# Kernel tuning notes

Hardware: AMD Instinct MI355X
Metric: run time of the kernel (lower is better)

## Reference

```python
import jax, jax.numpy as jnp
import numpy as np

N = 50000
E = 800000
IN = 256
HID = 64
HEADS = 4
EPS = 1e-5


def batchnorm(x, g, b):
    # training-mode BatchNorm1d over node dim, biased variance (torch semantics)
    mu = jnp.mean(x, axis=0)
    var = jnp.mean((x - mu) ** 2, axis=0)
    return (x - mu) * jax.lax.rsqrt(var + EPS) * g + b


def gat(x, edge_index, W, a_src, a_dst, bias, heads, out_ch, num_nodes):
    src, dst = edge_index[0], edge_index[1]
    h = (x @ W).reshape(num_nodes, heads, out_ch)          # [N,H,C]
    al_s = jnp.einsum('nhc,hc->nh', h, a_src)              # [N,H]
    al_d = jnp.einsum('nhc,hc->nh', h, a_dst)
    e = jax.nn.leaky_relu(al_s[src] + al_d[dst], 0.2)      # [E,H]
    # segment softmax over destination neighborhoods
    m = jax.ops.segment_max(e, dst, num_segments=num_nodes)
    m = jnp.where(jnp.isfinite(m), m, 0.0)
    ex = jnp.exp(e - m[dst])                               # [E,H]
    denom = jax.ops.segment_sum(ex, dst, num_segments=num_nodes)
    alpha = ex / (denom[dst] + 1e-16)                      # [E,H]
    msg = alpha[:, :, None] * h[src]                       # [E,H,C]
    out = jax.ops.segment_sum(msg, dst, num_segments=num_nodes)
    return out.reshape(num_nodes, heads * out_ch) + bias


def setup_inputs() -> dict:
    key = jax.random.key(0)
    ks = jax.random.split(key, 12)
    d = {}
    d['x'] = jax.random.normal(ks[0], (N, IN), jnp.float32)
    d['edge_index'] = jax.random.randint(ks[1], (2, E), 0, N, jnp.int32)
    d['bn1_g'] = jnp.ones((IN,), jnp.float32)
    d['bn1_b'] = jnp.zeros((IN,), jnp.float32)
    d['lin1_W'] = jax.random.normal(ks[2], (IN, HID * HEADS), jnp.float32) * (1.0 / np.sqrt(IN))
    d['lin1_b'] = jnp.zeros((HID * HEADS,), jnp.float32)
    d['con1_W'] = jax.random.normal(ks[3], (IN, HID * HEADS), jnp.float32) * (1.0 / np.sqrt(IN))
    d['con1_asrc'] = jax.random.normal(ks[4], (HEADS, HID), jnp.float32) * 0.1
    d['con1_adst'] = jax.random.normal(ks[5], (HEADS, HID), jnp.float32) * 0.1
    d['con1_b'] = jnp.zeros((HID * HEADS,), jnp.float32)
    d['bn3_g'] = jnp.ones((HID * HEADS,), jnp.float32)
    d['bn3_b'] = jnp.zeros((HID * HEADS,), jnp.float32)
    d['lin3_W'] = jax.random.normal(ks[6], (HID * HEADS, 2), jnp.float32) * (1.0 / np.sqrt(HID * HEADS))
    d['lin3_b'] = jnp.zeros((2,), jnp.float32)
    d['con3_W'] = jax.random.normal(ks[7], (HID * HEADS, 2), jnp.float32) * (1.0 / np.sqrt(HID * HEADS))
    d['con3_asrc'] = jax.random.normal(ks[8], (1, 2), jnp.float32) * 0.1
    d['con3_adst'] = jax.random.normal(ks[9], (1, 2), jnp.float32) * 0.1
    d['con3_b'] = jnp.zeros((2,), jnp.float32)
    return d


def reference(x, edge_index, bn1_g, bn1_b, lin1_W, lin1_b, con1_W, con1_asrc, con1_adst, con1_b,
              bn3_g, bn3_b, lin3_W, lin3_b, con3_W, con3_asrc, con3_adst, con3_b):
    x = batchnorm(x, bn1_g, bn1_b)
    x = jax.nn.relu(x @ lin1_W + lin1_b
                    + gat(x, edge_index, con1_W, con1_asrc, con1_adst, con1_b, HEADS, HID, N))
    x = batchnorm(x, bn3_g, bn3_b)
    x = jax.nn.relu(x @ lin3_W + lin3_b
                    + gat(x, edge_index, con3_W, con3_asrc, con3_adst, con3_b, 1, 2, N))
    return x
```

## Files before the change

kernel.cpp:

```cpp
#include <hip/hip_runtime.h>
#include <math.h>

#define NN 50000
#define NE 800000
#define IC 256
#define EPS 1e-5f

typedef __attribute__((ext_vector_type(8))) short short8;
typedef __attribute__((ext_vector_type(4))) float f32x4;

enum : int {
  OFF_S1     = 0,
  OFF_S2     = 256,
  OFF_COUNTS = 512,
  ZERO_END   = OFF_COUNTS + 50000,
  OFF_CURSOR = ZERO_END,
  OFF_START  = OFF_CURSOR + 50000,
  OFF_BSUM   = OFF_START + 50004,
  OFF_BOFF   = OFF_BSUM + 64,
  OFF_ALS    = OFF_BOFF + 64,
  OFF_ALD    = OFF_ALS + 200000,
  OFF_SRCS   = OFF_ALD + 200000,
  OFF_Y32    = OFF_SRCS + 800000,
  OFF_ND4    = OFF_Y32 + 100000,
  OFF_BFH    = OFF_ND4 + 200000,
  OFF_HBF    = OFF_BFH + 65536,
  OFF_YLBF   = OFF_HBF + 6400000,
  WS_FLOATS  = OFF_YLBF + 6400000
};

__device__ __forceinline__ float lrelu(float s) { return s > 0.f ? s : 0.2f * s; }
__device__ __forceinline__ float b2f(unsigned short u) {
  return __uint_as_float(((unsigned)u) << 16);
}
__device__ __forceinline__ unsigned short f2bf(float f) {
  unsigned u = __float_as_uint(f);
  return (unsigned short)((u + 0x7fffu + ((u >> 16) & 1u)) >> 16);
}
__device__ __forceinline__ unsigned cvtpk(float lo, float hi) {
  unsigned r;
  asm("v_cvt_pk_bf16_f32 %0, %1, %2" : "=v"(r) : "v"(lo), "v"(hi));
  return r;
}

__global__ __launch_bounds__(256) void k_prep(const float* __restrict__ x,
                                              float* __restrict__ S1,
                                              float* __restrict__ S2,
                                              const int* __restrict__ dst,
                                              int* __restrict__ counts,
                                              const float* __restrict__ Wlin,
                                              const float* __restrict__ Wcon,
                                              unsigned short* __restrict__ Bfh) {
  int b = blockIdx.x;
  if (b < 1024) {
    int c = threadIdx.x;
    float s1 = 0.f, s2 = 0.f;
    for (int r = b; r < NN; r += 1024) {
      float v = x[r * IC + c];
      s1 += v;
      s2 = fmaf(v, v, s2);
    }
    atomicAdd(&S1[c], s1);
    atomicAdd(&S2[c], s2);
  } else if (b < 4149) {
    int e = (b - 1024) * 256 + threadIdx.x;
    atomicAdd(&counts[dst[e]], 1);
  } else {
    int id = (b - 4149) * 256 + threadIdx.x;
    int j = id & 7, lane = (id >> 3) & 63, nt = (id >> 9) & 31, ks = id >> 14;
    int k = ks * 32 + ((lane >> 4) << 3) + j;
    int n = nt * 16 + (lane & 15);
    float v = (n < 256) ? Wlin[k * 256 + n] : Wcon[k * 256 + (n - 256)];
    Bfh[id] = f2bf(v);
  }
}

__global__ __launch_bounds__(256) void k_bnstats2(const unsigned short* __restrict__ x1,
                                                  float* __restrict__ S1,
                                                  float* __restrict__ S2) {
  int c = threadIdx.x;
  float s1 = 0.f, s2 = 0.f;
  for (int r = blockIdx.x; r < NN; r += gridDim.x) {
    float v = b2f(x1[r * IC + c]);
    s1 += v;
    s2 = fmaf(v, v, s2);
  }
  atomicAdd(&S1[c], s1);
  atomicAdd(&S2[c], s2);
}

__global__ __launch_bounds__(256, 4) void k_gemm(const float* __restrict__ x,
                                                 const float* __restrict__ S1,
                                                 const float* __restrict__ S2,
                                                 const float* __restrict__ bng,
                                                 const float* __restrict__ bnb,
                                                 const unsigned short* __restrict__ Bfh,
                                                 unsigned short* __restrict__ ylbf,
                                                 unsigned short* __restrict__ hbf,
                                                 const float* __restrict__ asrc,
                                                 const float* __restrict__ adst,
                                                 float* __restrict__ als,
                                                 float* __restrict__ ald,
                                                 const int* __restrict__ counts,
                                                 int* __restrict__ start,
                                                 int* __restrict__ cursor) {
  const int tid = threadIdx.x;
  const int b = blockIdx.x;
  if (b < 56) {
    if (b >= 49) return;
    __shared__ int red[4], wsum[4];
    const int lane = tid & 63, wv = tid >> 6;
    const int base = b << 10;
    int pre = 0;
    for (int i = tid; i < base; i += 256) pre += counts[i];
#pragma unroll
    for (int off = 1; off < 64; off <<= 1) pre += __shfl_xor(pre, off, 64);
    if (lane == 0) red[wv] = pre;
    const int i0 = base + tid * 4;
    int c0 = (i0 < NN) ? counts[i0] : 0;
    int c1 = (i0 + 1 < NN) ? counts[i0 + 1] : 0;
    int c2 = (i0 + 2 < NN) ? counts[i0 + 2] : 0;
    int c3 = (i0 + 3 < NN) ? counts[i0 + 3] : 0;
    const int tsum = c0 + c1 + c2 + c3;
    int isc = tsum;
#pragma unroll
    for (int off = 1; off < 64; off <<= 1) {
      int t = __shfl_up(isc, off, 64);
      if (lane >= off) isc += t;
    }
    if (lane == 63) wsum[wv] = isc;
    __syncthreads();
    int ex = red[0] + red[1] + red[2] + red[3] + (isc - tsum);
    for (int w = 0; w < wv; ++w) ex += wsum[w];
    if (i0 < NN) { start[i0] = ex; cursor[i0] = ex; }
    ex += c0;
    if (i0 + 1 < NN) { start[i0 + 1] = ex; cursor[i0 + 1] = ex; }
    ex += c1;
    if (i0 + 2 < NN) { start[i0 + 2] = ex; cursor[i0 + 2] = ex; }
    ex += c2;
    if (i0 + 3 < NN) { start[i0 + 3] = ex; cursor[i0 + 3] = ex; }
    ex += c3;
    if (b == 48 && tid == 255) start[NN] = ex;
    return;
  }
  const int g = b - 56;
  const int row_blk = (g >> 4) * 8 + (g & 7);
  const int bn = (g >> 3) & 1;
  if (row_blk >= 782) return;
  const int row0 = row_blk * 64;
  __shared__ unsigned short Ah[2048];
  __shared__ float sc[256], sh[256];
  const int wave = tid >> 6, lane = tid & 63;
  {
    float mu = S1[tid] * (1.f / NN);
    float var = S2[tid] * (1.f / NN) - mu * mu;
    float ss = bng[tid] / sqrtf(var + EPS);
    sc[tid] = ss;
    sh[tid] = bnb[tid] - mu * ss;
  }
  const float4* x4 = (const float4*)x;
  const short8* Bh8 = (const short8*)Bfh;
  f32x4 acc[4][4];
#pragma unroll
  for (int i = 0; i < 4; ++i)
#pragma unroll
    for (int j = 0; j < 4; ++j) acc[i][j] = (f32x4){0.f, 0.f, 0.f, 0.f};

  const int m = tid >> 2, kg = tid & 3;
  const int r = row0 + m;
  const int aaddr = (((m >> 4) * 64) + ((m & 15) | (kg << 4))) * 8;
  __syncthreads();

  for (int ks = 0; ks < 8; ++ks) {
    const int c0 = ks * 32 + kg * 8;
    float v[8];
    if (r < NN) {
      int base = (r * IC + c0) >> 2;
      float4 fa = x4[base], fb = x4[base + 1];
      v[0] = fa.x; v[1] = fa.y; v[2] = fa.z; v[3] = fa.w;
      v[4] = fb.x; v[5] = fb.y; v[6] = fb.z; v[7] = fb.w;
#pragma unroll
      for (int j = 0; j < 8; ++j) v[j] = fmaf(v[j], sc[c0 + j], sh[c0 + j]);
    } else {
#pragma unroll
      for (int j = 0; j < 8; ++j) v[j] = 0.f;
    }
    unsigned ph[4];
#pragma unroll
    for (int j = 0; j < 4; ++j) ph[j] = cvtpk(v[2 * j], v[2 * j + 1]);
    *(uint4*)&Ah[aaddr] = make_uint4(ph[0], ph[1], ph[2], ph[3]);
    __syncthreads();

    short8 ah[4];
#pragma unroll
    for (int mt = 0; mt < 4; ++mt)
      ah[mt] = *(const short8*)&Ah[(mt * 64 + lane) * 8];
#pragma unroll
    for (int nt = 0; nt < 4; ++nt) {
      short8 bh = Bh8[(ks * 32 + bn * 16 + wave * 4 + nt) * 64 + lane];
#pragma unroll
      for (int mt = 0; mt < 4; ++mt)
        acc[mt][nt] = __builtin_amdgcn_mfma_f32_16x16x32_bf16(ah[mt], bh, acc[mt][nt], 0, 0, 0);
    }
    __syncthreads();
  }
  const int colq = lane & 15, quad = lane >> 4;
  if (bn == 0) {
#pragma unroll
    for (int mt = 0; mt < 4; ++mt)
#pragma unroll
      for (int reg = 0; reg < 4; ++reg) {
        int rr = row0 + mt * 16 + quad * 4 + reg;
        if (rr < NN) {
#pragma unroll
          for (int nt = 0; nt < 4; ++nt)
            ylbf[rr * IC + wave * 64 + nt * 16 + colq] = f2bf(acc[mt][nt][reg]);
        }
      }
  } else {
    const int head = wave;
    float asv[4], adv[4];
#pragma unroll
    for (int j = 0; j < 4; ++j) {
      asv[j] = asrc[head * 64 + j * 16 + colq];
      adv[j] = adst[head * 64 + j * 16 + colq];
    }
#pragma unroll
    for (int mt = 0; mt < 4; ++mt)
#pragma unroll
      for (int reg = 0; reg < 4; ++reg) {
        int rr = row0 + mt * 16 + quad * 4 + reg;
        float sA = 0.f, dA = 0.f;
#pragma unroll
        for (int j = 0; j < 4; ++j) {
          float hA = acc[mt][j][reg];
          sA = fmaf(hA, asv[j], sA);
          dA = fmaf(hA, adv[j], dA);
          if (rr < NN) hbf[rr * IC + head * 64 + j * 16 + colq] = f2bf(hA);
        }
#pragma unroll
        for (int off = 1; off < 16; off <<= 1) {
          sA += __shfl_xor(sA, off, 64);
          dA += __shfl_xor(dA, off, 64);
        }
        if (rr < NN) {
          if (colq == 0) als[rr * 4 + head] = sA;
          else if (colq == 1) ald[rr * 4 + head] = dA;
        }
      }
  }
}

__global__ __launch_bounds__(256) void k_scatter(const int* __restrict__ src,
                                                 const int* __restrict__ dst,
                                                 int* __restrict__ cursor,
                                                 int* __restrict__ srcs,
                                                 float* __restrict__ S1,
                                                 float* __restrict__ S2) {
  if (blockIdx.x == 0) {
    S1[threadIdx.x] = 0.f;
    S2[threadIdx.x] = 0.f;
  }
  int e = blockIdx.x * 256 + threadIdx.x;
  int pos = atomicAdd(&cursor[dst[e]], 1);
  srcs[pos] = src[e];
}

__global__ __launch_bounds__(256) void k_agg(const ushort4* __restrict__ hq,
                                             ushort4* __restrict__ x1,
                                             const float4* __restrict__ als4,
                                             const float4* __restrict__ ald4,
                                             const int* __restrict__ start,
                                             const int* __restrict__ srcs,
                                             const float4* __restrict__ lb4,
                                             const float4* __restrict__ cb4,
                                             const int nb0) {
  __shared__ float lsp[1024];
  const int tid = threadIdx.x;
  const int wave = tid >> 6, lane = tid & 63, head = lane >> 4;
  const int n = nb0 + blockIdx.x * 4 + wave;
  const float* als = (const float*)als4;
  const int s = start[n], t = start[n + 1];
  const int deg = t - s;
  const float4 aldv = ald4[n];
  int svk = -1;
  float p0 = 0.f, p1 = 0.f, p2 = 0.f, p3 = 0.f;
  if (lane < deg) {
    svk = srcs[s + lane];
    float4 a = als4[svk];
    p0 = __expf(lrelu(a.x + aldv.x));
    p1 = __expf(lrelu(a.y + aldv.y));
    p2 = __expf(lrelu(a.z + aldv.z));
    p3 = __expf(lrelu(a.w + aldv.w));
  }
  *(float4*)&lsp[wave * 256 + lane * 4] = make_float4(p0, p1, p2, p3);
  float d0 = p0, d1 = p1, d2 = p2, d3 = p3;
  const float aldh = head == 0 ? aldv.x : head == 1 ? aldv.y : head == 2 ? aldv.z : aldv.w;
  if (deg > 64) {
    for (int i = s + 64 + lane; i < t; i += 64) {
      float4 a = als4[srcs[i]];
      d0 += __expf(lrelu(a.x + aldv.x));
      d1 += __expf(lrelu(a.y + aldv.y));
      d2 += __expf(lrelu(a.z + aldv.z));
      d3 += __expf(lrelu(a.w + aldv.w));
    }
  }
#pragma unroll
  for (int off = 1; off < 64; off <<= 1) {
    d0 += __shfl_xor(d0, off, 64);
    d1 += __shfl_xor(d1, off, 64);
    d2 += __shfl_xor(d2, off, 64);
    d3 += __shfl_xor(d3, off, 64);
  }
  const float inv =
      1.f / ((head == 0 ? d0 : head == 1 ? d1 : head == 2 ? d2 : d3) + 1e-16f);
  float a0 = 0.f, a1 = 0.f, a2 = 0.f, a3 = 0.f;
  const int cnt = min(deg, 64);
  const int wbase = wave * 256 + head;
  int j = 0;
  for (; j + 4 <= cnt; j += 4) {
    int sv0 = __shfl(svk, j, 64), sv1 = __shfl(svk, j + 1, 64);
    int sv2 = __shfl(svk, j + 2, 64), sv3 = __shfl(svk, j + 3, 64);
    ushort4 hv0 = hq[sv0 * 64 + lane];
    ushort4 hv1 = hq[sv1 * 64 + lane];
    ushort4 hv2 = hq[sv2 * 64 + lane];
    ushort4 hv3 = hq[sv3 * 64 + lane];
    float w0 = lsp[wbase + j * 4], w1 = lsp[wbase + j * 4 + 4];
    float w2 = lsp[wbase + j * 4 + 8], w3 = lsp[wbase + j * 4 + 12];
    a0 = fmaf(w0, b2f(hv0.x), a0); a1 = fmaf(w0, b2f(hv0.y), a1);
    a2 = fmaf(w0, b2f(hv0.z), a2); a3 = fmaf(w0, b2f(hv0.w), a3);
    a0 = fmaf(w1, b2f(hv1.x), a0); a1 = fmaf(w1, b2f(hv1.y), a1);
    a2 = fmaf(w1, b2f(hv1.z), a2); a3 = fmaf(w1, b2f(hv1.w), a3);
    a0 = fmaf(w2, b2f(hv2.x), a0); a1 = fmaf(w2, b2f(hv2.y), a1);
    a2 = fmaf(w2, b2f(hv2.z), a2); a3 = fmaf(w2, b2f(hv2.w), a3);
    a0 = fmaf(w3, b2f(hv3.x), a0); a1 = fmaf(w3, b2f(hv3.y), a1);
    a2 = fmaf(w3, b2f(hv3.z), a2); a3 = fmaf(w3, b2f(hv3.w), a3);
  }
  for (; j < cnt; ++j) {
    int sv = __shfl(svk, j, 64);
    float w = lsp[wbase + j * 4];
    ushort4 hv = hq[sv * 64 + lane];
    a0 = fmaf(w, b2f(hv.x), a0);
    a1 = fmaf(w, b2f(hv.y), a1);
    a2 = fmaf(w, b2f(hv.z), a2);
    a3 = fmaf(w, b2f(hv.w), a3);
  }
  if (deg > 64) {
    for (int i = s + 64; i < t; ++i) {
      int sv = srcs[i];
      float av = als[sv * 4 + head];
      float p = __expf(lrelu(av + aldh));
      ushort4 hv = hq[sv * 64 + lane];
      a0 = fmaf(p, b2f(hv.x), a0);
      a1 = fmaf(p, b2f(hv.y), a1);
      a2 = fmaf(p, b2f(hv.z), a2);
      a3 = fmaf(p, b2f(hv.w), a3);
    }
  }
  ushort4 yb = x1[n * 64 + lane];
  float4 bb1 = lb4[lane], bb2 = cb4[lane];
  ushort4 rb;
  rb.x = f2bf(fmaxf(fmaf(a0, inv, b2f(yb.x) + bb1.x + bb2.x), 0.f));
  rb.y = f2bf(fmaxf(fmaf(a1, inv, b2f(yb.y) + bb1.y + bb2.y), 0.f));
  rb.z = f2bf(fmaxf(fmaf(a2, inv, b2f(yb.z) + bb1.z + bb2.z), 0.f));
  rb.w = f2bf(fmaxf(fmaf(a3, inv, b2f(yb.w) + bb1.w + bb2.w), 0.f));
  x1[n * 64 + lane] = rb;
}

__global__ __launch_bounds__(256) void k_node2(const ushort4* __restrict__ x1,
                                               const float* __restrict__ S1,
                                               const float* __restrict__ S2,
                                               const float* __restrict__ g3,
                                               const float* __restrict__ b3,
                                               const float4* __restrict__ Wl4,
                                               const float4* __restrict__ Wc4,
                                               const float* __restrict__ a3s,
                                               const float* __restrict__ a3d,
                                               const float* __restrict__ l3b,
                                               const float* __restrict__ c3b,
                                               float2* __restrict__ y32,
                                               float4* __restrict__ nd4) {
  __shared__ float sc[256], sh[256];
  const int tid = threadIdx.x;
  {
    float mu = S1[tid] * (1.f / NN);
    float var = S2[tid] * (1.f / NN) - mu * mu;
    float ss = g3[tid] / sqrtf(var + EPS);
    sc[tid] = ss;
    sh[tid] = b3[tid] - mu * ss;
  }
  __syncthreads();
  const int n = blockIdx.x * 4 + (tid >> 6);
  const int lane = tid & 63;
  ushort4 xb = x1[n * 64 + lane];
  float x0 = fmaf(b2f(xb.x), sc[lane * 4 + 0], sh[lane * 4 + 0]);
  float x1v = fmaf(b2f(xb.y), sc[lane * 4 + 1], sh[lane * 4 + 1]);
  float x2 = fmaf(b2f(xb.z), sc[lane * 4 + 2], sh[lane * 4 + 2]);
  float x3 = fmaf(b2f(xb.w), sc[lane * 4 + 3], sh[lane * 4 + 3]);
  float4 wa = Wl4[lane * 2], wb = Wl4[lane * 2 + 1];
  float y0 = x0 * wa.x + x1v * wa.z + x2 * wb.x + x3 * wb.z;
  float y1 = x0 * wa.y + x1v * wa.w + x2 * wb.y + x3 * wb.w;
  float4 ca = Wc4[lane * 2], cb = Wc4[lane * 2 + 1];
  float g0 = x0 * ca.x + x1v * ca.z + x2 * cb.x + x3 * cb.z;
  float g1 = x0 * ca.y + x1v * ca.w + x2 * cb.y + x3 * cb.w;
#pragma unroll
  for (int off = 1; off < 64; off <<= 1) {
    y0 += __shfl_xor(y0, off, 64);
    y1 += __shfl_xor(y1, off, 64);
    g0 += __shfl_xor(g0, off, 64);
    g1 += __shfl_xor(g1, off, 64);
  }
  if (lane == 0) {
    y32[n] = make_float2(y0 + l3b[0] + c3b[0], y1 + l3b[1] + c3b[1]);
    nd4[n] = make_float4(g0 * a3s[0] + g1 * a3s[1], g0, g1,
                         g0 * a3d[0] + g1 * a3d[1]);
  }
}

__global__ __launch_bounds__(256) void k_final(const int* __restrict__ start,
                                               const int* __restrict__ srcs,
                                               const float4* __restrict__ nd4,
                                               const float2* __restrict__ y32,
                                               float* __restrict__ out) {
  const int tid = threadIdx.x;
  const int n = blockIdx.x * 16 + (tid >> 4);
  const int li = tid & 15;
  const int s = start[n], t = start[n + 1];
  const float ad = nd4[n].w;
  float den = 0.f, a0 = 0.f, a1 = 0.f;
  for (int ii = s + li; ii < t; ii += 16) {
    float4 vv = nd4[srcs[ii]];
    float p = __expf(lrelu(vv.x + ad));
    den += p;
    a0 = fmaf(p, vv.y, a0);
    a1 = fmaf(p, vv.z, a1);
  }
#pragma unroll
  for (int off = 1; off < 16; off <<= 1) {
    den += __shfl_xor(den, off, 64);
    a0 += __shfl_xor(a0, off, 64);
    a1 += __shfl_xor(a1, off, 64);
  }
  if (li == 0) {
    float2 y = y32[n];
    float inv = 1.f / (den + 1e-16f);
    out[2 * n] = fmaxf(fmaf(a0, inv, y.x), 0.f);
    out[2 * n + 1] = fmaxf(fmaf(a1, inv, y.y), 0.f);
  }
}

extern "C" void kernel_launch(void* const* d_in, const int* in_sizes, int n_in,
                              void* d_out, int out_size, void* d_ws, size_t ws_size,
                              hipStream_t stream) {
  const float* x = (const float*)d_in[0];
  const int* ei = (const int*)d_in[1];
  const float* bn1_g = (const float*)d_in[2];
  const float* bn1_b = (const float*)d_in[3];
  const float* lin1_W = (const float*)d_in[4];
  const float* lin1_b = (const float*)d_in[5];
  const float* con1_W = (const float*)d_in[6];
  const float* con1_as = (const float*)d_in[7];
  const float* con1_ad = (const float*)d_in[8];
  const float* con1_b = (const float*)d_in[9];
  const float* bn3_g = (const float*)d_in[10];
  const float* bn3_b = (const float*)d_in[11];
  const float* lin3_W = (const float*)d_in[12];
  const float* lin3_b = (const float*)d_in[13];
  const float* con3_W = (const float*)d_in[14];
  const float* con3_as = (const float*)d_in[15];
  const float* con3_ad = (const float*)d_in[16];
  const float* con3_b = (const float*)d_in[17];
  float* ws = (float*)d_ws;
  const int* srcA = ei;
  const int* dstA = ei + NE;

  float* S1 = ws + OFF_S1;
  float* S2 = ws + OFF_S2;
  int* counts = (int*)(ws + OFF_COUNTS);
  int* cursor = (int*)(ws + OFF_CURSOR);
  int* start = (int*)(ws + OFF_START);
  float* als = ws + OFF_ALS;
  float* ald = ws + OFF_ALD;
  int* srcs = (int*)(ws + OFF_SRCS);
  float2* y32 = (float2*)(ws + OFF_Y32);
  float4* nd4 = (float4*)(ws + OFF_ND4);
  unsigned short* Bfh = (unsigned short*)(ws + OFF_BFH);
  unsigned short* hbf = (unsigned short*)(ws + OFF_HBF);
  unsigned short* ylbf = (unsigned short*)(ws + OFF_YLBF);

  hipMemsetAsync(ws, 0, (size_t)ZERO_END * sizeof(float), stream);

  k_prep<<<4661, 256, 0, stream>>>(x, S1, S2, dstA, counts, lin1_W, con1_W, Bfh);
  k_gemm<<<56 + 1568, 256, 0, stream>>>(x, S1, S2, bn1_g, bn1_b, Bfh, ylbf, hbf,
                                        con1_as, con1_ad, als, ald, counts, start,
                                        cursor);
  k_scatter<<<3125, 256, 0, stream>>>(srcA, dstA, cursor, srcs, S1, S2);
  k_agg<<<6250, 256, 0, stream>>>((const ushort4*)hbf, (ushort4*)ylbf,
                                  (const float4*)als, (const float4*)ald, start,
                                  srcs, (const float4*)lin1_b,
                                  (const float4*)con1_b, 0);
  k_agg<<<6250, 256, 0, stream>>>((const ushort4*)hbf, (ushort4*)ylbf,
                                  (const float4*)als, (const float4*)ald, start,
                                  srcs, (const float4*)lin1_b,
                                  (const float4*)con1_b, 25000);
  k_bnstats2<<<1024, 256, 0, stream>>>(ylbf, S1, S2);
  k_node2<<<12500, 256, 0, stream>>>((const ushort4*)ylbf, S1, S2, bn3_g, bn3_b,
                                     (const float4*)lin3_W, (const float4*)con3_W,
                                     con3_as, con3_ad, lin3_b, con3_b, y32, nd4);
  k_final<<<3125, 256, 0, stream>>>(start, srcs, nd4, y32, (float*)d_out);
}
```

Baseline: 407.7 us.

## Replace scatter-time atomics with privatized 8-way counts and per-edge ranks

Degree counting now uses 8 privatized count arrays selected by block index, and records each edge's rank from the atomicAdd return value. The scan builds per-copy offsets, so the scatter computes positions directly without a second round of atomics on the cursor. This aims to reduce atomic contention and drop the atomics from the scatter. In exchange the scan reads 8x more count data, the memset zeroes a larger region, and an extra byte-per-edge rank array is stored. The bnstats2 grid is also halved.

```diff
diff --git a/kernel.cpp b/kernel.cpp
--- a/kernel.cpp
+++ b/kernel.cpp
@@ -5,6 +5,7 @@
 #define NE 800000
 #define IC 256
 #define EPS 1e-5f
+#define P8 50176
 
 typedef __attribute__((ext_vector_type(8))) short short8;
 typedef __attribute__((ext_vector_type(4))) float f32x4;
@@ -12,13 +13,12 @@
 enum : int {
   OFF_S1     = 0,
   OFF_S2     = 256,
-  OFF_COUNTS = 512,
-  ZERO_END   = OFF_COUNTS + 50000,
-  OFF_CURSOR = ZERO_END,
-  OFF_START  = OFF_CURSOR + 50000,
-  OFF_BSUM   = OFF_START + 50004,
-  OFF_BOFF   = OFF_BSUM + 64,
-  OFF_ALS    = OFF_BOFF + 64,
+  OFF_C8     = 512,
+  ZERO_END   = OFF_C8 + 8 * P8,
+  OFF_COFF   = ZERO_END,
+  OFF_START  = OFF_COFF + 8 * P8,
+  OFF_RANK   = OFF_START + 50004,
+  OFF_ALS    = OFF_RANK + 200000,
   OFF_ALD    = OFF_ALS + 200000,
   OFF_SRCS   = OFF_ALD + 200000,
   OFF_Y32    = OFF_SRCS + 800000,
@@ -47,7 +47,8 @@
                                               float* __restrict__ S1,
                                               float* __restrict__ S2,
                                               const int* __restrict__ dst,
-                                              int* __restrict__ counts,
+                                              int* __restrict__ counts8,
+                                              unsigned char* __restrict__ rank8,
                                               const float* __restrict__ Wlin,
                                               const float* __restrict__ Wcon,
                                               unsigned short* __restrict__ Bfh) {
@@ -64,7 +65,9 @@
     atomicAdd(&S2[c], s2);
   } else if (b < 4149) {
     int e = (b - 1024) * 256 + threadIdx.x;
-    atomicAdd(&counts[dst[e]], 1);
+    int copy = b & 7;
+    int old = atomicAdd(&counts8[copy * P8 + dst[e]], 1);
+    rank8[e] = (unsigned char)old;
   } else {
     int id = (b - 4149) * 256 + threadIdx.x;
     int j = id & 7, lane = (id >> 3) & 63, nt = (id >> 9) & 31, ks = id >> 14;
@@ -101,9 +104,9 @@
                                                  const float* __restrict__ adst,
                                                  float* __restrict__ als,
                                                  float* __restrict__ ald,
-                                                 const int* __restrict__ counts,
-                                                 int* __restrict__ start,
-                                                 int* __restrict__ cursor) {
+                                                 const int* __restrict__ counts8,
+                                                 int* __restrict__ coff,
+                                                 int* __restrict__ start) {
   const int tid = threadIdx.x;
   const int b = blockIdx.x;
   if (b < 56) {
@@ -112,16 +115,31 @@
     const int lane = tid & 63, wv = tid >> 6;
     const int base = b << 10;
     int pre = 0;
-    for (int i = tid; i < base; i += 256) pre += counts[i];
+    for (int i = tid; i < base; i += 256) {
+      int s = 0;
+#pragma unroll
+      for (int k = 0; k < 8; ++k) s += counts8[k * P8 + i];
+      pre += s;
+    }
 #pragma unroll
     for (int off = 1; off < 64; off <<= 1) pre += __shfl_xor(pre, off, 64);
     if (lane == 0) red[wv] = pre;
     const int i0 = base + tid * 4;
-    int c0 = (i0 < NN) ? counts[i0] : 0;
-    int c1 = (i0 + 1 < NN) ? counts[i0 + 1] : 0;
-    int c2 = (i0 + 2 < NN) ? counts[i0 + 2] : 0;
-    int c3 = (i0 + 3 < NN) ? counts[i0 + 3] : 0;
-    const int tsum = c0 + c1 + c2 + c3;
+    int pc[8][4];
+#pragma unroll
+    for (int k = 0; k < 8; ++k) {
+      int4 v = *(const int4*)&counts8[k * P8 + i0];
+      pc[k][0] = v.x; pc[k][1] = v.y; pc[k][2] = v.z; pc[k][3] = v.w;
+    }
+    int tot[4];
+#pragma unroll
+    for (int j = 0; j < 4; ++j) {
+      int s = 0;
+#pragma unroll
+      for (int k = 0; k < 8; ++k) s += pc[k][j];
+      tot[j] = s;
+    }
+    const int tsum = tot[0] + tot[1] + tot[2] + tot[3];
     int isc = tsum;
 #pragma unroll
     for (int off = 1; off < 64; off <<= 1) {
@@ -132,14 +150,18 @@
     __syncthreads();
     int ex = red[0] + red[1] + red[2] + red[3] + (isc - tsum);
     for (int w = 0; w < wv; ++w) ex += wsum[w];
-    if (i0 < NN) { start[i0] = ex; cursor[i0] = ex; }
-    ex += c0;
-    if (i0 + 1 < NN) { start[i0 + 1] = ex; cursor[i0 + 1] = ex; }
-    ex += c1;
-    if (i0 + 2 < NN) { start[i0 + 2] = ex; cursor[i0 + 2] = ex; }
-    ex += c2;
-    if (i0 + 3 < NN) { start[i0 + 3] = ex; cursor[i0 + 3] = ex; }
-    ex += c3;
+#pragma unroll
+    for (int j = 0; j < 4; ++j) {
+      const int i = i0 + j;
+      int run = ex;
+#pragma unroll
+      for (int k = 0; k < 8; ++k) {
+        coff[k * P8 + i] = run;
+        run += pc[k][j];
+      }
+      if (i < NN) start[i] = ex;
+      ex += tot[j];
+    }
     if (b == 48 && tid == 255) start[NN] = ex;
     return;
   }
@@ -253,7 +275,8 @@
 
 __global__ __launch_bounds__(256) void k_scatter(const int* __restrict__ src,
                                                  const int* __restrict__ dst,
-                                                 int* __restrict__ cursor,
+                                                 const int* __restrict__ coff,
+                                                 const unsigned char* __restrict__ rank8,
                                                  int* __restrict__ srcs,
                                                  float* __restrict__ S1,
                                                  float* __restrict__ S2) {
@@ -262,7 +285,8 @@
     S2[threadIdx.x] = 0.f;
   }
   int e = blockIdx.x * 256 + threadIdx.x;
-  int pos = atomicAdd(&cursor[dst[e]], 1);
+  int copy = blockIdx.x & 7;
+  int pos = coff[copy * P8 + dst[e]] + (int)rank8[e];
   srcs[pos] = src[e];
 }
 
@@ -476,9 +500,10 @@
 
   float* S1 = ws + OFF_S1;
   float* S2 = ws + OFF_S2;
-  int* counts = (int*)(ws + OFF_COUNTS);
-  int* cursor = (int*)(ws + OFF_CURSOR);
+  int* counts8 = (int*)(ws + OFF_C8);
+  int* coff = (int*)(ws + OFF_COFF);
   int* start = (int*)(ws + OFF_START);
+  unsigned char* rank8 = (unsigned char*)(ws + OFF_RANK);
   float* als = ws + OFF_ALS;
   float* ald = ws + OFF_ALD;
   int* srcs = (int*)(ws + OFF_SRCS);
@@ -490,11 +515,12 @@
 
   hipMemsetAsync(ws, 0, (size_t)ZERO_END * sizeof(float), stream);
 
-  k_prep<<<4661, 256, 0, stream>>>(x, S1, S2, dstA, counts, lin1_W, con1_W, Bfh);
+  k_prep<<<4661, 256, 0, stream>>>(x, S1, S2, dstA, counts8, rank8, lin1_W,
+                                   con1_W, Bfh);
   k_gemm<<<56 + 1568, 256, 0, stream>>>(x, S1, S2, bn1_g, bn1_b, Bfh, ylbf, hbf,
-                                        con1_as, con1_ad, als, ald, counts, start,
-                                        cursor);
-  k_scatter<<<3125, 256, 0, stream>>>(srcA, dstA, cursor, srcs, S1, S2);
+                                        con1_as, con1_ad, als, ald, counts8,
+                                        coff, start);
+  k_scatter<<<3125, 256, 0, stream>>>(srcA, dstA, coff, rank8, srcs, S1, S2);
   k_agg<<<6250, 256, 0, stream>>>((const ushort4*)hbf, (ushort4*)ylbf,
                                   (const float4*)als, (const float4*)ald, start,
                                   srcs, (const float4*)lin1_b,
@@ -503,7 +529,7 @@
                                   (const float4*)als, (const float4*)ald, start,
                                   srcs, (const float4*)lin1_b,
                                   (const float4*)con1_b, 25000);
-  k_bnstats2<<<1024, 256, 0, stream>>>(ylbf, S1, S2);
+  k_bnstats2<<<512, 256, 0, stream>>>(ylbf, S1, S2);
   k_node2<<<12500, 256, 0, stream>>>((const ushort4*)ylbf, S1, S2, bn3_g, bn3_b,
                                      (const float4*)lin3_W, (const float4*)con3_W,
                                      con3_as, con3_ad, lin3_b, con3_b, y32, nd4);
```

After: 428.5 us. +5.1%, slower.
